# Kernel optimization log

Measured on AMD Instinct MI355X. Metric: run time of the kernel, lower is better.

## Reference

```python
import jax, jax.numpy as jnp
import numpy as np

OMEGA = 1.0
EPS = 1e-05
B, N = 4096, 4096  # batch x landmarks -> 16.7M 2x2 eigenproblems


def setup_inputs() -> dict:
    key = jax.random.key(0)
    kp, kc, kt = jax.random.split(key, 3)
    pred = jax.random.normal(kp, (B, N, 2), dtype=jnp.float32)
    A = jax.random.normal(kc, (B, N, 2, 2), dtype=jnp.float32)
    # symmetric PSD covariance with eigenvalues bounded away from 0
    cov = A @ jnp.swapaxes(A, -1, -2) + 0.1 * jnp.eye(2, dtype=jnp.float32)
    target = jax.random.normal(kt, (B, N, 2), dtype=jnp.float32)
    return {"pred": pred, "cov": cov, "target": target}


def _star_loss(pred, cov, target):
    # closed-form eigendecomposition of symmetric 2x2 [[a, b], [b, d]]
    a = cov[..., 0, 0]
    b = cov[..., 0, 1]
    d = cov[..., 1, 1]
    mean = 0.5 * (a + d)
    delta = jnp.sqrt((0.5 * (a - d)) ** 2 + b * b)
    lam1 = mean + delta  # larger eigenvalue
    lam2 = mean - delta  # smaller eigenvalue
    # eigenvector for lam1: [b, lam1 - a]; diagonal fallback when b ~ 0
    diag = jnp.abs(b) < 1e-12
    vx = jnp.where(diag, jnp.where(a >= d, 1.0, 0.0), b)
    vy = jnp.where(diag, jnp.where(a >= d, 0.0, 1.0), lam1 - a)
    inv_n = 1.0 / jnp.sqrt(vx * vx + vy * vy)
    vx = vx * inv_n
    vy = vy * inv_n
    # projection residuals along the two (orthonormal) eigen-directions
    dx = pred[..., 0] - target[..., 0]
    dy = pred[..., 1] - target[..., 1]
    # distance='l2' with reduction='sum' over ALL elements -> scalar dists,
    # exactly matching F.mse_loss(..., reduction='sum') in the torch code
    d1 = jnp.sum((vx * dx + vy * dy) ** 2)
    d2 = jnp.sum((-vy * dx + vx * dy) ** 2)
    loss = (1.0 / jnp.sqrt(lam1) + EPS) * d1 \
         + (1.0 / jnp.sqrt(lam2) + EPS) * d2 \
         + 0.5 * OMEGA * (lam1 + lam2)  # regularizer = omega/2 * trace
    return jnp.mean(loss)  # reduction='mean'


def reference(pred, cov, target):
    return _star_loss(pred, cov, target)
```

## Files before the change

### kernel.cpp

```cpp
#include <hip/hip_runtime.h>


#define NBLOCKS  4096
#define NTHREADS 256
#define NACC     5
#define M_ELEMS  16777216
#define STRIDE   (NBLOCKS * NTHREADS)
#define STEPS    (M_ELEMS / STRIDE)
#define UNROLL   4
#define EPS      1e-5
#define OMEGA    1.0

typedef float f4 __attribute__((ext_vector_type(4)));
typedef float f2 __attribute__((ext_vector_type(2)));

__device__ __forceinline__ f4 nt_load4(const f4* p) {
    return __builtin_nontemporal_load(p);
}
__device__ __forceinline__ f2 nt_load2(const f2* p) {
    return __builtin_nontemporal_load(p);
}

__device__ __forceinline__ float wave_reduce_f(float v) {
    #pragma unroll
    for (int off = 32; off > 0; off >>= 1) v += __shfl_down(v, off, 64);
    return v;
}

__device__ __forceinline__ void star_elem(
    f4 c, float dx, float dy,
    float& s1, float& s2, float& s3, float& s4, float& s5)
{
    const float a = c.x, b = c.y, d = c.w;
    float mean  = 0.5f * (a + d);
    float hd    = 0.5f * (a - d);
    float delta = sqrtf(hd * hd + b * b);
    float lam1  = mean + delta;
    float lam2  = mean - delta;

    bool diag = fabsf(b) < 1e-12f;
    bool a_ge = (a >= d);
    float vx = diag ? (a_ge ? 1.0f : 0.0f) : b;
    float vy = diag ? (a_ge ? 0.0f : 1.0f) : (lam1 - a);
    float inv_n = rsqrtf(vx * vx + vy * vy);
    vx *= inv_n;
    vy *= inv_n;

    float r1 = vx * dx + vy * dy;
    float r2 = vx * dy - vy * dx;

    s1 += r1 * r1;
    s2 += r2 * r2;
    s3 += rsqrtf(lam1);
    s4 += rsqrtf(lam2);
    s5 += a + d;
}

__global__ __launch_bounds__(NTHREADS) void star_partial(
    const f2* __restrict__ pred,
    const f4* __restrict__ cov,
    const f2* __restrict__ tgt,
    float* __restrict__ partials)
{
    float s1 = 0.f, s2 = 0.f, s3 = 0.f, s4 = 0.f, s5 = 0.f;
    const int tid = blockIdx.x * NTHREADS + threadIdx.x;

    #pragma unroll 1
    for (int g = 0; g < STEPS; g += UNROLL) {
        f4 c[UNROLL];
        f2 p[UNROLL], t[UNROLL];
        #pragma unroll
        for (int u = 0; u < UNROLL; ++u) {
            const int e = (g + u) * STRIDE + tid;
            c[u] = nt_load4(&cov[e]);
            p[u] = nt_load2(&pred[e]);
            t[u] = nt_load2(&tgt[e]);
        }
        #pragma unroll
        for (int u = 0; u < UNROLL; ++u)
            star_elem(c[u], p[u].x - t[u].x, p[u].y - t[u].y,
                      s1, s2, s3, s4, s5);
    }

    float v[NACC] = {s1, s2, s3, s4, s5};
    #pragma unroll
    for (int k = 0; k < NACC; ++k) v[k] = wave_reduce_f(v[k]);

    __shared__ float red[NTHREADS / 64][NACC];
    const int lane = threadIdx.x & 63;
    const int wid  = threadIdx.x >> 6;
    if (lane == 0) {
        #pragma unroll
        for (int k = 0; k < NACC; ++k) red[wid][k] = v[k];
    }
    __syncthreads();
    if (threadIdx.x == 0) {
        #pragma unroll
        for (int k = 0; k < NACC; ++k) {
            float acc = 0.f;
            #pragma unroll
            for (int w = 0; w < NTHREADS / 64; ++w) acc += red[w][k];
            partials[blockIdx.x * NACC + k] = acc;
        }
    }
}

__global__ __launch_bounds__(NTHREADS) void star_final(
    const float* __restrict__ partials, float* __restrict__ out, int nblocks)
{
    double acc[NACC] = {0, 0, 0, 0, 0};
    for (int i = threadIdx.x; i < nblocks; i += NTHREADS) {
        #pragma unroll
        for (int k = 0; k < NACC; ++k) acc[k] += (double)partials[i * NACC + k];
    }

    #pragma unroll
    for (int k = 0; k < NACC; ++k) {
        #pragma unroll
        for (int off = 32; off > 0; off >>= 1)
            acc[k] += __shfl_down(acc[k], off, 64);
    }

    __shared__ double red[NTHREADS / 64][NACC];
    const int lane = threadIdx.x & 63;
    const int wid  = threadIdx.x >> 6;
    if (lane == 0) {
        #pragma unroll
        for (int k = 0; k < NACC; ++k) red[wid][k] = acc[k];
    }
    __syncthreads();

    if (threadIdx.x == 0) {
        double S[NACC];
        #pragma unroll
        for (int k = 0; k < NACC; ++k) {
            double t = 0.0;
            #pragma unroll
            for (int w = 0; w < NTHREADS / 64; ++w) t += red[w][k];
            S[k] = t;
        }
        const double M  = (double)M_ELEMS;
        const double S3 = S[2] + M * EPS;
        const double S4 = S[3] + M * EPS;
        double loss = (S[0] * S3 + S[1] * S4 + 0.5 * OMEGA * S[4]) / M;
        out[0] = (float)loss;
    }
}

extern "C" void kernel_launch(void* const* d_in, const int* in_sizes, int n_in,
                              void* d_out, int out_size, void* d_ws, size_t ws_size,
                              hipStream_t stream) {
    const f2* pred = (const f2*)d_in[0];
    const f4* cov  = (const f4*)d_in[1];
    const f2* tgt  = (const f2*)d_in[2];
    float* out      = (float*)d_out;
    float* partials = (float*)d_ws;

    star_partial<<<NBLOCKS, NTHREADS, 0, stream>>>(pred, cov, tgt, partials);
    star_final<<<1, NTHREADS, 0, stream>>>(partials, out, NBLOCKS);
}
```

Measured before the change: 482.0 us.

## Stage inputs through LDS with direct global-to-LDS loads, double-buffered per wave

Replaces the grid-strided register loads with per-wave contiguous chunks that are copied straight into LDS using global_load_lds. Each wave has two buffers, so the load of the next 64-element tile overlaps with computing the current one, synchronised by manual s_waitcnt. pred and tgt are fetched as 16-byte vectors, with half the lanes loading each, to widen the transactions. This adds LDS traffic and occupancy pressure from 16KB of LDS per block, and relies on hand-written vmcnt accounting being correct.

```diff
diff --git a/kernel.cpp b/kernel.cpp
--- a/kernel.cpp
+++ b/kernel.cpp
@@ -3,28 +3,33 @@
 
 #define NBLOCKS  4096
 #define NTHREADS 256
+#define WAVES    (NTHREADS / 64)
 #define NACC     5
 #define M_ELEMS  16777216
-#define STRIDE   (NBLOCKS * NTHREADS)
-#define STEPS    (M_ELEMS / STRIDE)
-#define UNROLL   4
+#define EPW      (M_ELEMS / (NBLOCKS * WAVES))
+#define ITERS    (EPW / 64)
+#define BUFB     2048
 #define EPS      1e-5
 #define OMEGA    1.0
 
 typedef float f4 __attribute__((ext_vector_type(4)));
 typedef float f2 __attribute__((ext_vector_type(2)));
 
-__device__ __forceinline__ f4 nt_load4(const f4* p) {
-    return __builtin_nontemporal_load(p);
-}
-__device__ __forceinline__ f2 nt_load2(const f2* p) {
-    return __builtin_nontemporal_load(p);
+__device__ __forceinline__ void gload16(const void* g, void* l) {
+    __builtin_amdgcn_global_load_lds(
+        (const __attribute__((address_space(1))) void*)g,
+        (__attribute__((address_space(3))) void*)l, 16, 0, 0);
 }
 
-__device__ __forceinline__ float wave_reduce_f(float v) {
-    #pragma unroll
-    for (int off = 32; off > 0; off >>= 1) v += __shfl_down(v, off, 64);
-    return v;
+__device__ __forceinline__ void stage(
+    char* buf, const f4* __restrict__ cov,
+    const f4* __restrict__ pred4, const f4* __restrict__ tgt4,
+    int ebase, int lane)
+{
+    gload16(&cov[ebase + lane], buf);
+    const int pb = (ebase >> 1) + (lane & 31);
+    const f4* s = (lane < 32) ? &pred4[pb] : &tgt4[pb];
+    gload16(s, buf + 1024);
 }
 
 __device__ __forceinline__ void star_elem(
@@ -56,39 +61,62 @@
     s5 += a + d;
 }
 
+__device__ __forceinline__ void consume(
+    const char* buf, int lane,
+    float& s1, float& s2, float& s3, float& s4, float& s5)
+{
+    f4 c = ((const f4*)(buf))[lane];
+    f2 p = ((const f2*)(buf + 1024))[lane];
+    f2 t = ((const f2*)(buf + 1536))[lane];
+    star_elem(c, p.x - t.x, p.y - t.y, s1, s2, s3, s4, s5);
+}
+
+__device__ __forceinline__ float wave_reduce_f(float v) {
+    #pragma unroll
+    for (int off = 32; off > 0; off >>= 1) v += __shfl_down(v, off, 64);
+    return v;
+}
+
 __global__ __launch_bounds__(NTHREADS) void star_partial(
     const f2* __restrict__ pred,
     const f4* __restrict__ cov,
     const f2* __restrict__ tgt,
     float* __restrict__ partials)
 {
+    __shared__ __align__(16) char lds[WAVES][2][BUFB];
+
     float s1 = 0.f, s2 = 0.f, s3 = 0.f, s4 = 0.f, s5 = 0.f;
-    const int tid = blockIdx.x * NTHREADS + threadIdx.x;
+    const int lane = threadIdx.x & 63;
+    const int wid  = threadIdx.x >> 6;
+    const int wbase = (blockIdx.x * WAVES + wid) * EPW;
 
-    #pragma unroll 1
-    for (int g = 0; g < STEPS; g += UNROLL) {
-        f4 c[UNROLL];
-        f2 p[UNROLL], t[UNROLL];
-        #pragma unroll
-        for (int u = 0; u < UNROLL; ++u) {
-            const int e = (g + u) * STRIDE + tid;
-            c[u] = nt_load4(&cov[e]);
-            p[u] = nt_load2(&pred[e]);
-            t[u] = nt_load2(&tgt[e]);
+    const f4* pred4 = (const f4*)pred;
+    const f4* tgt4  = (const f4*)tgt;
+
+    char* buf0 = &lds[wid][0][0];
+    char* buf1 = &lds[wid][1][0];
+
+    stage(buf0, cov, pred4, tgt4, wbase, lane);
+
+    #pragma unroll
+    for (int it = 0; it < ITERS; it += 2) {
+        stage(buf1, cov, pred4, tgt4, wbase + (it + 1) * 64, lane);
+        asm volatile("s_waitcnt vmcnt(2)" ::: "memory");
+        consume(buf0, lane, s1, s2, s3, s4, s5);
+        if (it + 2 < ITERS) {
+            stage(buf0, cov, pred4, tgt4, wbase + (it + 2) * 64, lane);
+            asm volatile("s_waitcnt vmcnt(2)" ::: "memory");
+        } else {
+            asm volatile("s_waitcnt vmcnt(0)" ::: "memory");
         }
-        #pragma unroll
-        for (int u = 0; u < UNROLL; ++u)
-            star_elem(c[u], p[u].x - t[u].x, p[u].y - t[u].y,
-                      s1, s2, s3, s4, s5);
+        consume(buf1, lane, s1, s2, s3, s4, s5);
     }
 
     float v[NACC] = {s1, s2, s3, s4, s5};
     #pragma unroll
     for (int k = 0; k < NACC; ++k) v[k] = wave_reduce_f(v[k]);
 
-    __shared__ float red[NTHREADS / 64][NACC];
-    const int lane = threadIdx.x & 63;
-    const int wid  = threadIdx.x >> 6;
+    __shared__ float red[WAVES][NACC];
     if (lane == 0) {
         #pragma unroll
         for (int k = 0; k < NACC; ++k) red[wid][k] = v[k];
@@ -99,7 +127,7 @@
         for (int k = 0; k < NACC; ++k) {
             float acc = 0.f;
             #pragma unroll
-            for (int w = 0; w < NTHREADS / 64; ++w) acc += red[w][k];
+            for (int w = 0; w < WAVES; ++w) acc += red[w][k];
             partials[blockIdx.x * NACC + k] = acc;
         }
     }
```

Result: slower. 506.5 us (+5.1%).
